# Kernel tuning notes

Hardware: AMD Instinct MI355X
Metric: run time of the kernel (lower is better)

Reference implementation:

```python
import jax, jax.numpy as jnp
import numpy as np

B, N, V, H = 8, 2048, 256, 1024
EPS = 1e-5
NEG = -1e9


def _layernorm(x, g, b):
    m = jnp.mean(x, axis=-1, keepdims=True)
    v = jnp.mean((x - m) ** 2, axis=-1, keepdims=True)
    return (x - m) / jnp.sqrt(v + EPS) * g + b


def setup_inputs() -> dict:
    key = jax.random.key(0)
    ks = jax.random.split(key, 10)
    tril = jnp.tril(jnp.ones((N, N), jnp.float32))
    return {
        "h": jax.random.normal(ks[0], (B, N, V), jnp.float32),
        "mask_one": tril,                      # keep causal entries
        "mask_zero": NEG * (1.0 - tril),       # -inf-ish above diagonal
        "ln_attn_g": jnp.ones((V,), jnp.float32),
        "ln_attn_b": jnp.zeros((V,), jnp.float32),
        "ln_mlp_g": jnp.ones((V,), jnp.float32),
        "ln_mlp_b": jnp.zeros((V,), jnp.float32),
        "wv": jax.random.normal(ks[1], (V,), jnp.float32),
        "wv_bos": jax.random.normal(ks[2], (V,), jnp.float32),
        "wo_w": jax.random.normal(ks[3], (V, V), jnp.float32) / np.sqrt(V),
        "qk_bos": jax.random.normal(ks[4], (V,), jnp.float32),
        "qk_previous": jax.random.normal(ks[5], (V,), jnp.float32),
        "qk_direction": jnp.ones((V,), jnp.float32),  # middel_layer=False, frozen
        "w1": jax.random.normal(ks[6], (H, V), jnp.float32) / np.sqrt(V),
        "w2": jax.random.normal(ks[7], (V, H), jnp.float32) / np.sqrt(H),
    }


def reference(h, mask_one, mask_zero, ln_attn_g, ln_attn_b, ln_mlp_g, ln_mlp_b,
              wv, wv_bos, wo_w, qk_bos, qk_previous, qk_direction, w1, w2):
    b, n, v = h.shape
    # mask blends LayerNorm only into row 0 (BOS position)
    attn_input = h.at[:, 0, :].set(_layernorm(h[:, 0, :], ln_attn_g, ln_attn_b))
    # value states: diag(wv) on positions 1.., wo(wv_bos) at position 0
    values = attn_input[:, 1:, :] * wv                      # [B, N-1, V]
    v_bos = wo_w @ wv_bos                                   # Linear(bias=False)
    values = jnp.concatenate(
        [jnp.broadcast_to(v_bos, (b, 1, v)), values], axis=1)  # [B, N, V]
    # sparse QK logits: column 0 term + sub-diagonal term, densified then masked
    col0 = (attn_input @ qk_bos) * (attn_input[:, 0, :] @ qk_direction)[:, None]  # [B, N]
    d = attn_input @ qk_previous                            # [B, N]
    qk = jnp.zeros((b, n, n), h.dtype).at[:, :, 0].add(col0)
    idx = jnp.arange(1, n)
    qk = qk.at[:, idx, idx - 1].add(d[:, 1:])               # row r, col r-1 = d[:, r]
    qk = qk * mask_one + mask_zero
    attn_out = jax.nn.softmax(qk, axis=-1) @ values         # [B, N, V]
    # FFN branch with its own BOS-only LayerNorm blend
    mlp_input = h.at[:, 0, :].set(_layernorm(h[:, 0, :], ln_mlp_g, ln_mlp_b))
    mlp_out = jax.nn.relu(mlp_input @ w1.T) @ w2.T          # [B, N, V]
    return attn_out + mlp_out
```

## Files before the change

### kernel.cpp

```cpp
#include <hip/hip_runtime.h>
#include <hip/hip_bf16.h>

#define BB 8
#define NN 2048
#define VV 256
#define HH 1024
#define CHK 64
#define RPC 32
constexpr float EPS = 1e-5f;

typedef __attribute__((ext_vector_type(4))) float floatx4;
typedef __attribute__((ext_vector_type(8))) short short8;

__device__ __forceinline__ void load_lds16(const void* g, void* l) {
    __builtin_amdgcn_global_load_lds((const __attribute__((address_space(1))) void*)g,
                                     (__attribute__((address_space(3))) void*)l, 16, 0, 0);
}
__device__ __forceinline__ float bf16s_to_f(short s) {
    unsigned u = ((unsigned)(unsigned short)s) << 16;
    return __builtin_bit_cast(float, u);
}

__global__ void prep_kernel(const float* __restrict__ h,
                            const float* __restrict__ g_attn, const float* __restrict__ b_attn,
                            const float* __restrict__ g_mlp,  const float* __restrict__ b_mlp,
                            const float* __restrict__ qk_dir,
                            const float* __restrict__ wo_w,  const float* __restrict__ wv_bos,
                            float* __restrict__ attn_row0, float* __restrict__ mlp_row0,
                            float* __restrict__ v_bos, float* __restrict__ sum0)
{
    int t = threadIdx.x;
    __shared__ float red[VV];
    if (blockIdx.x < BB) {
        int b = blockIdx.x;
        float x = h[(size_t)b * NN * VV + t];
        red[t] = x; __syncthreads();
        for (int s = 128; s > 0; s >>= 1) { if (t < s) red[t] += red[t + s]; __syncthreads(); }
        float m = red[0] * (1.0f / VV); __syncthreads();
        float xc = x - m;
        red[t] = xc * xc; __syncthreads();
        for (int s = 128; s > 0; s >>= 1) { if (t < s) red[t] += red[t + s]; __syncthreads(); }
        float var = red[0] * (1.0f / VV); __syncthreads();
        float inv = 1.0f / sqrtf(var + EPS);
        float an = xc * inv * g_attn[t] + b_attn[t];
        float mn = xc * inv * g_mlp[t] + b_mlp[t];
        attn_row0[b * VV + t] = an;
        mlp_row0[b * VV + t]  = mn;
        red[t] = an * qk_dir[t]; __syncthreads();
        for (int s = 128; s > 0; s >>= 1) { if (t < s) red[t] += red[t + s]; __syncthreads(); }
        if (t == 0) sum0[b] = red[0];
    } else {
        const float4* wp = reinterpret_cast<const float4*>(wo_w + (size_t)t * VV);
        const float4* vp = reinterpret_cast<const float4*>(wv_bos);
        float acc = 0.f;
        for (int j = 0; j < VV / 4; ++j) {
            float4 a = wp[j], b = vp[j];
            acc += a.x * b.x + a.y * b.y + a.z * b.z + a.w * b.w;
        }
        v_bos[t] = acc;
    }
}

__global__ __launch_bounds__(256) void scan_qkw_cvt_kernel(
    const float* __restrict__ h, const float* __restrict__ mlp_row0,
    const float* __restrict__ wv,
    const float* __restrict__ qk_bos, const float* __restrict__ qk_prev,
    const float* __restrict__ sum0,
    short* __restrict__ Xb,
    float* __restrict__ w0, float* __restrict__ wprev, float* __restrict__ wz,
    float* __restrict__ chunkSum)
{
    __shared__ float lds[4][VV];
    int wave = threadIdx.x >> 6, lane = threadIdx.x & 63;
    int b = blockIdx.x / CHK, c = blockIdx.x % CHK;
    int r0 = c * RPC + wave * 8;
    float4 wv4 = reinterpret_cast<const float4*>(wv)[lane];
    float4 qb4 = reinterpret_cast<const float4*>(qk_bos)[lane];
    float4 qp4 = reinterpret_cast<const float4*>(qk_prev)[lane];
    float s0b = sum0[b];
    float4 vsum = {0.f, 0.f, 0.f, 0.f};
#pragma unroll
    for (int rr = 0; rr < 8; ++rr) {
        int r = r0 + rr;
        size_t base = ((size_t)b * NN + r) * VV;
        float4 x = *reinterpret_cast<const float4*>(h + base + lane * 4);
        float4 xs = x;
        if (r == 0) xs = *reinterpret_cast<const float4*>(mlp_row0 + b * VV + lane * 4);
        __hip_bfloat16 c0 = __float2bfloat16(xs.x), c1 = __float2bfloat16(xs.y),
                       c2 = __float2bfloat16(xs.z), c3 = __float2bfloat16(xs.w);
        short4 pk;
        pk.x = *reinterpret_cast<short*>(&c0);
        pk.y = *reinterpret_cast<short*>(&c1);
        pk.z = *reinterpret_cast<short*>(&c2);
        pk.w = *reinterpret_cast<short*>(&c3);
        *reinterpret_cast<short4*>(Xb + base + lane * 4) = pk;
        if (r != 0) {
            vsum.x += bf16s_to_f(pk.x) * wv4.x; vsum.y += bf16s_to_f(pk.y) * wv4.y;
            vsum.z += bf16s_to_f(pk.z) * wv4.z; vsum.w += bf16s_to_f(pk.w) * wv4.w;
        }
        float s1 = x.x * qb4.x + x.y * qb4.y + x.z * qb4.z + x.w * qb4.w;
        float s2 = x.x * qp4.x + x.y * qp4.y + x.z * qp4.z + x.w * qp4.w;
        for (int off = 32; off > 0; off >>= 1) {
            s1 += __shfl_down(s1, off);
            s2 += __shfl_down(s2, off);
        }
        if (lane == 0) {
            int gid = b * NN + r;
            float W0, WP, WZ;
            if (r == 0) { W0 = 1.f; WP = 0.f; WZ = 0.f; }
            else if (r == 1) {
                float a = s1 * s0b + s2;
                float m = fmaxf(a, 0.f);
                float ea = expf(a - m), ez = expf(-m);
                float Z = ea + ez;
                W0 = ea / Z; WZ = ez / Z; WP = WZ;
            } else {
                float a = s1 * s0b;
                float m = fmaxf(fmaxf(a, s2), 0.f);
                float ea = expf(a - m), ed = expf(s2 - m), ez = expf(-m);
                float Z = ea + ed + (float)(r - 1) * ez;
                W0 = ea / Z; WP = ed / Z; WZ = ez / Z;
            }
            w0[gid] = W0; wprev[gid] = WP; wz[gid] = WZ;
        }
    }
    reinterpret_cast<float4*>(lds[wave])[lane] = vsum;
    __syncthreads();
    int v = threadIdx.x;
    chunkSum[((size_t)b * CHK + c) * VV + v] = lds[0][v] + lds[1][v] + lds[2][v] + lds[3][v];
}

__global__ void chunkscan_kernel(float* __restrict__ chunkSum)
{
    int b = blockIdx.x, v = threadIdx.x;
    float vals[CHK];
#pragma unroll
    for (int c = 0; c < CHK; ++c) vals[c] = chunkSum[(b * CHK + c) * VV + v];
    float run = 0.f;
#pragma unroll
    for (int c = 0; c < CHK; ++c) { float t = vals[c]; vals[c] = run; run += t; }
#pragma unroll
    for (int c = 0; c < CHK; ++c) chunkSum[(b * CHK + c) * VV + v] = vals[c];
}

__global__ __launch_bounds__(128) void attn_kernel(
    const short* __restrict__ Xb, const float* __restrict__ wv,
    const float* __restrict__ v_bos,
    const float* __restrict__ w0, const float* __restrict__ wprev,
    const float* __restrict__ wz, const float* __restrict__ chunkSum,
    float* __restrict__ out)
{
    int b = blockIdx.x / CHK, c = blockIdx.x % CHK;
    int v = threadIdx.x * 2;
    float2 wv2 = *reinterpret_cast<const float2*>(wv + v);
    float2 vb2 = *reinterpret_cast<const float2*>(v_bos + v);
    float2 S = *reinterpret_cast<const float2*>(chunkSum + (b * CHK + c) * VV + v);
    int r0 = c * RPC;
    float2 prev = {0.f, 0.f};
    if (r0 > 0) {
        short2 p = *reinterpret_cast<const short2*>(Xb + ((size_t)b * NN + r0 - 1) * VV + v);
        prev.x = bf16s_to_f(p.x) * wv2.x; prev.y = bf16s_to_f(p.y) * wv2.y;
    }
    for (int r = r0; r < r0 + RPC; ++r) {
        size_t idx = ((size_t)b * NN + r) * VV + v;
        float2 o;
        if (r == 0) {
            o = vb2;
            prev.x = 0.f; prev.y = 0.f;
        } else {
            short2 xv = *reinterpret_cast<const short2*>(Xb + idx);
            float2 val;
            val.x = bf16s_to_f(xv.x) * wv2.x; val.y = bf16s_to_f(xv.y) * wv2.y;
            S.x += val.x; S.y += val.y;
            int wi = b * NN + r;
            float W0 = w0[wi], WD = wprev[wi] - wz[wi], WZ = wz[wi];
            o.x = W0 * vb2.x + WD * prev.x + WZ * S.x;
            o.y = W0 * vb2.y + WD * prev.y + WZ * S.y;
            prev = val;
        }
        *reinterpret_cast<float2*>(out + idx) = o;
    }
}

__global__ void cvt_w_kernel(const float* __restrict__ w1, const float* __restrict__ w2,
                             __hip_bfloat16* __restrict__ w1b, __hip_bfloat16* __restrict__ w2b)
{
    int i = (blockIdx.x * blockDim.x + threadIdx.x) * 4;
    const float* src;
    __hip_bfloat16* dst;
    if (i < HH * VV) { src = w1 + i; dst = w1b + i; }
    else             { src = w2 + (i - HH * VV); dst = w2b + (i - HH * VV); }
    float4 x = *reinterpret_cast<const float4*>(src);
    dst[0] = __float2bfloat16(x.x);
    dst[1] = __float2bfloat16(x.y);
    dst[2] = __float2bfloat16(x.z);
    dst[3] = __float2bfloat16(x.w);
}

__global__ __launch_bounds__(512) void mlp_fused3(const short* __restrict__ Xb,
                                                  const short* __restrict__ w1b,
                                                  const short* __restrict__ w2b,
                                                  float* __restrict__ out)
{
    __shared__ __align__(16) short sW1[2][64 * 256];
    __shared__ __align__(16) short sW2[2][256 * 64];
    __shared__ __align__(16) short sY[64 * 64];
    int wave = threadIdx.x >> 6, lane = threadIdx.x & 63;
    int wm = wave >> 2, wn = wave & 3;
    int ra = lane & 15, q = lane >> 4;
    int m0 = blockIdx.x * 64;

    short8 xf[8][2];
#pragma unroll
    for (int ks = 0; ks < 8; ++ks)
#pragma unroll
        for (int i = 0; i < 2; ++i)
            xf[ks][i] = *reinterpret_cast<const short8*>(
                Xb + (size_t)(m0 + wm * 32 + i * 16 + ra) * VV + ks * 32 + q * 8);

    floatx4 oacc[2][4];
#pragma unroll
    for (int i = 0; i < 2; ++i)
#pragma unroll
        for (int j = 0; j < 4; ++j) oacc[i][j] = floatx4{0.f, 0.f, 0.f, 0.f};

    auto stage = [&](int hc, int buf) {
#pragma unroll
        for (int it = 0; it < 4; ++it) {
            int g = wave * 4 + it;
            int n = g * 2 + (lane >> 5);
            int slot = lane & 31;
            load_lds16(w1b + (size_t)(hc * 64 + n) * VV + (slot ^ (n & 7)) * 8,
                       &sW1[buf][g * 512]);
        }
#pragma unroll
        for (int it = 0; it < 4; ++it) {
            int g = wave * 4 + it;
            int v = g * 8 + (lane >> 3);
            int slot = lane & 7;
            load_lds16(w2b + (size_t)v * HH + hc * 64 + (slot ^ (v & 7)) * 8,
                       &sW2[buf][g * 512]);
        }
    };

    stage(0, 0);
    for (int hc = 0; hc < 16; ++hc) {
        int p = hc & 1;
        __syncthreads();
        if (hc < 15) stage(hc + 1, p ^ 1);

        floatx4 yacc[2];
        yacc[0] = floatx4{0.f, 0.f, 0.f, 0.f};
        yacc[1] = floatx4{0.f, 0.f, 0.f, 0.f};
        int nb = wn * 16 + ra;
#pragma unroll
        for (int ks = 0; ks < 8; ++ks) {
            short8 bfr = *reinterpret_cast<const short8*>(
                &sW1[p][nb * 256 + (((ks * 4 + q) ^ (ra & 7)) * 8)]);
#pragma unroll
            for (int i = 0; i < 2; ++i)
                yacc[i] = __builtin_amdgcn_mfma_f32_16x16x32_bf16(xf[ks][i], bfr, yacc[i], 0, 0, 0);
        }
#pragma unroll
        for (int i = 0; i < 2; ++i)
#pragma unroll
            for (int reg = 0; reg < 4; ++reg) {
                int m = wm * 32 + i * 16 + q * 4 + reg;
                int ke = wn * 16 + ra;
                __hip_bfloat16 hb = __float2bfloat16(fmaxf(yacc[i][reg], 0.f));
                sY[m * 64 + (((ke >> 3) ^ (m & 7)) * 8) + (ke & 7)] =
                    *reinterpret_cast<short*>(&hb);
            }
        __syncthreads();

#pragma unroll
        for (int kk = 0; kk < 2; ++kk) {
            short8 a2[2];
#pragma unroll
            for (int i = 0; i < 2; ++i) {
                int m = wm * 32 + i * 16 + ra;
                a2[i] = *reinterpret_cast<const short8*>(
                    &sY[m * 64 + (((kk * 4 + q) ^ (ra & 7)) * 8)]);
            }
#pragma unroll
            for (int j = 0; j < 4; ++j) {
                int v = wn * 64 + j * 16 + ra;
                short8 b2 = *reinterpret_cast<const short8*>(
                    &sW2[p][v * 64 + (((kk * 4 + q) ^ (ra & 7)) * 8)]);
#pragma unroll
                for (int i = 0; i < 2; ++i)
                    oacc[i][j] = __builtin_amdgcn_mfma_f32_16x16x32_bf16(a2[i], b2, oacc[i][j], 0, 0, 0);
            }
        }
    }

#pragma unroll
    for (int i = 0; i < 2; ++i)
#pragma unroll
        for (int j = 0; j < 4; ++j)
#pragma unroll
            for (int reg = 0; reg < 4; ++reg) {
                int row = m0 + wm * 32 + i * 16 + q * 4 + reg;
                int col = wn * 64 + j * 16 + ra;
                out[(size_t)row * VV + col] += oacc[i][j][reg];
            }
}

extern "C" void kernel_launch(void* const* d_in, const int* in_sizes, int n_in,
                              void* d_out, int out_size, void* d_ws, size_t ws_size,
                              hipStream_t stream)
{
    const float* h        = (const float*)d_in[0];
    const float* ln_attn_g = (const float*)d_in[3];
    const float* ln_attn_b = (const float*)d_in[4];
    const float* ln_mlp_g  = (const float*)d_in[5];
    const float* ln_mlp_b  = (const float*)d_in[6];
    const float* wv        = (const float*)d_in[7];
    const float* wv_bos    = (const float*)d_in[8];
    const float* wo_w      = (const float*)d_in[9];
    const float* qk_bos    = (const float*)d_in[10];
    const float* qk_prev   = (const float*)d_in[11];
    const float* qk_dir    = (const float*)d_in[12];
    const float* w1        = (const float*)d_in[13];
    const float* w2        = (const float*)d_in[14];
    float* out = (float*)d_out;

    float* attn_row0 = (float*)d_ws;
    float* mlp_row0  = attn_row0 + BB * VV;
    float* v_bos     = mlp_row0 + BB * VV;
    float* sum0      = v_bos + VV;
    float* w0        = sum0 + 8;
    float* wprev     = w0 + BB * NN;
    float* wzz       = wprev + BB * NN;
    float* chunkSum  = wzz + BB * NN;
    short* Xb            = (short*)(chunkSum + BB * CHK * VV);
    __hip_bfloat16* w1b  = (__hip_bfloat16*)(Xb + (size_t)BB * NN * VV);
    __hip_bfloat16* w2b  = w1b + HH * VV;

    prep_kernel<<<BB + 1, 256, 0, stream>>>(h, ln_attn_g, ln_attn_b, ln_mlp_g, ln_mlp_b,
                                            qk_dir, wo_w, wv_bos,
                                            attn_row0, mlp_row0, v_bos, sum0);
    cvt_w_kernel<<<(2 * HH * VV / 4) / 256, 256, 0, stream>>>(w1, w2, w1b, w2b);
    scan_qkw_cvt_kernel<<<BB * CHK, 256, 0, stream>>>(h, mlp_row0, wv, qk_bos, qk_prev,
                                                      sum0, Xb, w0, wprev, wzz, chunkSum);
    chunkscan_kernel<<<BB, 256, 0, stream>>>(chunkSum);
    attn_kernel<<<BB * CHK, 128, 0, stream>>>(Xb, wv, v_bos, w0, wprev, wzz, chunkSum, out);
    mlp_fused3<<<256, 512, 0, stream>>>(Xb, (const short*)w1b, (const short*)w2b, out);
}
```

Measured before the change: 172.3 us.

## Fuse attention epilogue into MLP kernel and merge prep with weight conversion

Merges the weight bf16 conversion into the prep kernel. It also removes the separate chunk-scan and attention kernels and folds their work into the tail of the fused MLP kernel: each block recomputes its own chunk prefix, writes the attention rows to shared memory, and adds them when storing the MLP result. This drops three launches and the read-modify-write of the output. The W1/W2 prefetch for the next chunk now starts after the first barrier rather than at the top of the loop, which shortens the overlap of loads with the first GEMM. Recomputing prefix sums with a serial loop over up to 63 chunks adds latency to the block epilogue.

```diff
diff --git a/kernel.cpp b/kernel.cpp
--- a/kernel.cpp
+++ b/kernel.cpp
@@ -21,15 +21,30 @@
     return __builtin_bit_cast(float, u);
 }
 
-__global__ void prep_kernel(const float* __restrict__ h,
-                            const float* __restrict__ g_attn, const float* __restrict__ b_attn,
-                            const float* __restrict__ g_mlp,  const float* __restrict__ b_mlp,
-                            const float* __restrict__ qk_dir,
-                            const float* __restrict__ wo_w,  const float* __restrict__ wv_bos,
-                            float* __restrict__ attn_row0, float* __restrict__ mlp_row0,
-                            float* __restrict__ v_bos, float* __restrict__ sum0)
+__global__ void prep_cvt_kernel(const float* __restrict__ h,
+                                const float* __restrict__ g_attn, const float* __restrict__ b_attn,
+                                const float* __restrict__ g_mlp,  const float* __restrict__ b_mlp,
+                                const float* __restrict__ qk_dir,
+                                const float* __restrict__ wo_w,  const float* __restrict__ wv_bos,
+                                const float* __restrict__ w1, const float* __restrict__ w2,
+                                float* __restrict__ attn_row0, float* __restrict__ mlp_row0,
+                                float* __restrict__ v_bos, float* __restrict__ sum0,
+                                __hip_bfloat16* __restrict__ w1b, __hip_bfloat16* __restrict__ w2b)
 {
     int t = threadIdx.x;
+    if (blockIdx.x > BB) {
+        int i = ((blockIdx.x - BB - 1) * 256 + t) * 4;
+        const float* src;
+        __hip_bfloat16* dst;
+        if (i < HH * VV) { src = w1 + i; dst = w1b + i; }
+        else             { src = w2 + (i - HH * VV); dst = w2b + (i - HH * VV); }
+        float4 x = *reinterpret_cast<const float4*>(src);
+        dst[0] = __float2bfloat16(x.x);
+        dst[1] = __float2bfloat16(x.y);
+        dst[2] = __float2bfloat16(x.z);
+        dst[3] = __float2bfloat16(x.w);
+        return;
+    }
     __shared__ float red[VV];
     if (blockIdx.x < BB) {
         int b = blockIdx.x;
@@ -130,77 +145,13 @@
     chunkSum[((size_t)b * CHK + c) * VV + v] = lds[0][v] + lds[1][v] + lds[2][v] + lds[3][v];
 }
 
-__global__ void chunkscan_kernel(float* __restrict__ chunkSum)
-{
-    int b = blockIdx.x, v = threadIdx.x;
-    float vals[CHK];
-#pragma unroll
-    for (int c = 0; c < CHK; ++c) vals[c] = chunkSum[(b * CHK + c) * VV + v];
-    float run = 0.f;
-#pragma unroll
-    for (int c = 0; c < CHK; ++c) { float t = vals[c]; vals[c] = run; run += t; }
-#pragma unroll
-    for (int c = 0; c < CHK; ++c) chunkSum[(b * CHK + c) * VV + v] = vals[c];
-}
-
-__global__ __launch_bounds__(128) void attn_kernel(
-    const short* __restrict__ Xb, const float* __restrict__ wv,
-    const float* __restrict__ v_bos,
+__global__ __launch_bounds__(512, 1) void mlp_attn_fused(
+    const short* __restrict__ Xb,
+    const short* __restrict__ w1b, const short* __restrict__ w2b,
+    const float* __restrict__ wv, const float* __restrict__ v_bos,
     const float* __restrict__ w0, const float* __restrict__ wprev,
     const float* __restrict__ wz, const float* __restrict__ chunkSum,
     float* __restrict__ out)
-{
-    int b = blockIdx.x / CHK, c = blockIdx.x % CHK;
-    int v = threadIdx.x * 2;
-    float2 wv2 = *reinterpret_cast<const float2*>(wv + v);
-    float2 vb2 = *reinterpret_cast<const float2*>(v_bos + v);
-    float2 S = *reinterpret_cast<const float2*>(chunkSum + (b * CHK + c) * VV + v);
-    int r0 = c * RPC;
-    float2 prev = {0.f, 0.f};
-    if (r0 > 0) {
-        short2 p = *reinterpret_cast<const short2*>(Xb + ((size_t)b * NN + r0 - 1) * VV + v);
-        prev.x = bf16s_to_f(p.x) * wv2.x; prev.y = bf16s_to_f(p.y) * wv2.y;
-    }
-    for (int r = r0; r < r0 + RPC; ++r) {
-        size_t idx = ((size_t)b * NN + r) * VV + v;
-        float2 o;
-        if (r == 0) {
-            o = vb2;
-            prev.x = 0.f; prev.y = 0.f;
-        } else {
-            short2 xv = *reinterpret_cast<const short2*>(Xb + idx);
-            float2 val;
-            val.x = bf16s_to_f(xv.x) * wv2.x; val.y = bf16s_to_f(xv.y) * wv2.y;
-            S.x += val.x; S.y += val.y;
-            int wi = b * NN + r;
-            float W0 = w0[wi], WD = wprev[wi] - wz[wi], WZ = wz[wi];
-            o.x = W0 * vb2.x + WD * prev.x + WZ * S.x;
-            o.y = W0 * vb2.y + WD * prev.y + WZ * S.y;
-            prev = val;
-        }
-        *reinterpret_cast<float2*>(out + idx) = o;
-    }
-}
-
-__global__ void cvt_w_kernel(const float* __restrict__ w1, const float* __restrict__ w2,
-                             __hip_bfloat16* __restrict__ w1b, __hip_bfloat16* __restrict__ w2b)
-{
-    int i = (blockIdx.x * blockDim.x + threadIdx.x) * 4;
-    const float* src;
-    __hip_bfloat16* dst;
-    if (i < HH * VV) { src = w1 + i; dst = w1b + i; }
-    else             { src = w2 + (i - HH * VV); dst = w2b + (i - HH * VV); }
-    float4 x = *reinterpret_cast<const float4*>(src);
-    dst[0] = __float2bfloat16(x.x);
-    dst[1] = __float2bfloat16(x.y);
-    dst[2] = __float2bfloat16(x.z);
-    dst[3] = __float2bfloat16(x.w);
-}
-
-__global__ __launch_bounds__(512) void mlp_fused3(const short* __restrict__ Xb,
-                                                  const short* __restrict__ w1b,
-                                                  const short* __restrict__ w2b,
-                                                  float* __restrict__ out)
 {
     __shared__ __align__(16) short sW1[2][64 * 256];
     __shared__ __align__(16) short sW2[2][256 * 64];
@@ -230,7 +181,7 @@
             int g = wave * 4 + it;
             int n = g * 2 + (lane >> 5);
             int slot = lane & 31;
-            load_lds16(w1b + (size_t)(hc * 64 + n) * VV + (slot ^ (n & 7)) * 8,
+            load_lds16(w1b + (size_t)(hc * 64 + n) * VV + ((slot ^ (n & 7)) * 8),
                        &sW1[buf][g * 512]);
         }
 #pragma unroll
@@ -238,7 +189,7 @@
             int g = wave * 4 + it;
             int v = g * 8 + (lane >> 3);
             int slot = lane & 7;
-            load_lds16(w2b + (size_t)v * HH + hc * 64 + (slot ^ (v & 7)) * 8,
+            load_lds16(w2b + (size_t)v * HH + hc * 64 + ((slot ^ (v & 7)) * 8),
                        &sW2[buf][g * 512]);
         }
     };
@@ -247,7 +198,6 @@
     for (int hc = 0; hc < 16; ++hc) {
         int p = hc & 1;
         __syncthreads();
-        if (hc < 15) stage(hc + 1, p ^ 1);
 
         floatx4 yacc[2];
         yacc[0] = floatx4{0.f, 0.f, 0.f, 0.f};
@@ -273,6 +223,8 @@
             }
         __syncthreads();
 
+        if (hc < 15) stage(hc + 1, p ^ 1);
+
 #pragma unroll
         for (int kk = 0; kk < 2; ++kk) {
             short8 a2[2];
@@ -294,15 +246,59 @@
         }
     }
 
+    float* aY = reinterpret_cast<float*>(&sW1[0][0]);
+    int t = threadIdx.x;
+    if (t < 256) {
+        int ch = t >> 7;
+        int vp = (t & 127) * 2;
+        int b = m0 >> 11;
+        int rbase = m0 & (NN - 1);
+        int c_glob = (rbase >> 5) + ch;
+        float2 wv2 = *reinterpret_cast<const float2*>(wv + vp);
+        float2 vb2 = *reinterpret_cast<const float2*>(v_bos + vp);
+        float2 S = {0.f, 0.f};
+        for (int cc = 0; cc < c_glob; ++cc) {
+            float2 ps = *reinterpret_cast<const float2*>(chunkSum + (b * CHK + cc) * VV + vp);
+            S.x += ps.x; S.y += ps.y;
+        }
+        int r0 = c_glob * RPC;
+        float2 prev = {0.f, 0.f};
+        if (r0 > 0) {
+            short2 pv = *reinterpret_cast<const short2*>(Xb + ((size_t)b * NN + r0 - 1) * VV + vp);
+            prev.x = bf16s_to_f(pv.x) * wv2.x; prev.y = bf16s_to_f(pv.y) * wv2.y;
+        }
+        for (int rr = 0; rr < RPC; ++rr) {
+            int r = r0 + rr;
+            float2 o;
+            if (r == 0) {
+                o = vb2;
+                prev.x = 0.f; prev.y = 0.f;
+            } else {
+                short2 xv = *reinterpret_cast<const short2*>(Xb + ((size_t)b * NN + r) * VV + vp);
+                float2 val;
+                val.x = bf16s_to_f(xv.x) * wv2.x; val.y = bf16s_to_f(xv.y) * wv2.y;
+                S.x += val.x; S.y += val.y;
+                int wi = b * NN + r;
+                float W0 = w0[wi], WD = wprev[wi] - wz[wi], WZ = wz[wi];
+                o.x = W0 * vb2.x + WD * prev.x + WZ * S.x;
+                o.y = W0 * vb2.y + WD * prev.y + WZ * S.y;
+                prev = val;
+            }
+            int lrow = ch * RPC + rr;
+            *reinterpret_cast<float2*>(aY + lrow * VV + vp) = o;
+        }
+    }
+    __syncthreads();
+
 #pragma unroll
     for (int i = 0; i < 2; ++i)
 #pragma unroll
         for (int j = 0; j < 4; ++j)
 #pragma unroll
             for (int reg = 0; reg < 4; ++reg) {
-                int row = m0 + wm * 32 + i * 16 + q * 4 + reg;
+                int lrow = wm * 32 + i * 16 + q * 4 + reg;
                 int col = wn * 64 + j * 16 + ra;
-                out[(size_t)row * VV + col] += oacc[i][j][reg];
+                out[(size_t)(m0 + lrow) * VV + col] = oacc[i][j][reg] + aY[lrow * VV + col];
             }
 }
 
@@ -337,13 +333,12 @@
     __hip_bfloat16* w1b  = (__hip_bfloat16*)(Xb + (size_t)BB * NN * VV);
     __hip_bfloat16* w2b  = w1b + HH * VV;
 
-    prep_kernel<<<BB + 1, 256, 0, stream>>>(h, ln_attn_g, ln_attn_b, ln_mlp_g, ln_mlp_b,
-                                            qk_dir, wo_w, wv_bos,
-                                            attn_row0, mlp_row0, v_bos, sum0);
-    cvt_w_kernel<<<(2 * HH * VV / 4) / 256, 256, 0, stream>>>(w1, w2, w1b, w2b);
+    prep_cvt_kernel<<<BB + 1 + (2 * HH * VV / 4) / 256, 256, 0, stream>>>(
+        h, ln_attn_g, ln_attn_b, ln_mlp_g, ln_mlp_b, qk_dir, wo_w, wv_bos,
+        w1, w2, attn_row0, mlp_row0, v_bos, sum0, w1b, w2b);
     scan_qkw_cvt_kernel<<<BB * CHK, 256, 0, stream>>>(h, mlp_row0, wv, qk_bos, qk_prev,
                                                       sum0, Xb, w0, wprev, wzz, chunkSum);
-    chunkscan_kernel<<<BB, 256, 0, stream>>>(chunkSum);
-    attn_kernel<<<BB * CHK, 128, 0, stream>>>(Xb, wv, v_bos, w0, wprev, wzz, chunkSum, out);
-    mlp_fused3<<<256, 512, 0, stream>>>(Xb, (const short*)w1b, (const short*)w2b, out);
-}
+    mlp_attn_fused<<<256, 512, 0, stream>>>((const short*)Xb, (const short*)w1b,
+                                            (const short*)w2b, wv, v_bos,
+                                            w0, wprev, wzz, chunkSum, out);
+}
```

Result: slower. 178.1 us (+3.4%).
